# Kernel optimization log

Measured on AMD Instinct MI355X. Metric: run time of the kernel, lower is better.

Reference implementation:

```python
import jax, jax.numpy as jnp
import numpy as np

B, S, DIN, DOUT, A, T, H = 8, 1024, 1024, 1024, 4, 4, 8  # arity A, T cell types, hidden H


def setup_inputs() -> dict:
    key = jax.random.key(0)
    ks = jax.random.split(key, 6)
    x = jax.random.normal(ks[0], (B, S, DIN), jnp.float32)
    sc = 1.0 / np.sqrt(DIN).astype(np.float32)
    weight = jax.random.uniform(ks[1], (A * DOUT, DIN), jnp.float32, -sc, sc)
    bias = jax.random.uniform(ks[2], (A * DOUT,), jnp.float32, -sc, sc)
    # stacked per-cell-type MLP params: arity -> H -> 1 (tanh)
    cw1 = jax.random.normal(ks[3], (T, A, H), jnp.float32) / np.sqrt(A).astype(np.float32)
    cb1 = jnp.zeros((T, H), jnp.float32)
    cw2 = jax.random.normal(ks[4], (T, H), jnp.float32) / np.sqrt(H).astype(np.float32)
    cb2 = jnp.zeros((T,), jnp.float32)
    return {"x": x, "weight": weight, "bias": bias,
            "cw1": cw1, "cb1": cb1, "cw2": cw2, "cb2": cb2}


def reference(x, weight, bias, cw1, cb1, cw2, cb2):
    T_, A_, H_ = cw1.shape
    Dout = weight.shape[0] // A_
    G = Dout // T_  # neurons per cell type (cell_indices = contiguous blocks via np.repeat)
    # all_inputs = F.linear(input, weight, bias): (B, S, A*Dout)
    z = jnp.einsum('bsd,od->bso', x, weight) + bias
    # slice per-neuron arity chunks -> (B, S, T, G, A)
    z = z.reshape(z.shape[0], z.shape[1], T_, G, A_)
    # per-cell-type MLP applied to every neuron of that type (replaces Python loop)
    h = jnp.tanh(jnp.einsum('bstga,tah->bstgh', z, cw1) + cb1[:, None, :])
    o = jnp.einsum('bstgh,th->bstg', h, cw2) + cb2[:, None]
    # concat over neurons -> (B, S, Dout)
    return o.reshape(o.shape[0], o.shape[1], Dout)
```

## Files before the change

kernel.cpp:

```cpp
#include <hip/hip_runtime.h>


typedef __bf16 bf16x8 __attribute__((ext_vector_type(8)));
typedef float f32x4 __attribute__((ext_vector_type(4)));
typedef float f32x16 __attribute__((ext_vector_type(16)));

#define BM 256
#define BN 256
#define BK 64
#define KDIM 1024
#define NT 16
#define BUFB 65536
#define BBASE 32768
#define RS 321
#define XN8 (8192 * 1024 / 8)
#define WN8 (4096 * 1024 / 8)

__global__ __launch_bounds__(256) void cvt_bf16_kernel(
    const float* __restrict__ x, const float* __restrict__ w,
    __bf16* __restrict__ xb, __bf16* __restrict__ wb) {
    int i = blockIdx.x * 256 + threadIdx.x;
    const float* src;
    __bf16* dst;
    int j;
    if (i < XN8) { src = x; dst = xb; j = i; }
    else         { src = w; dst = wb; j = i - XN8; }
    const f32x4* p = (const f32x4*)src + 2 * (size_t)j;
    f32x4 a = p[0], b = p[1];
    bf16x8 o;
    o[0] = (__bf16)a[0]; o[1] = (__bf16)a[1]; o[2] = (__bf16)a[2]; o[3] = (__bf16)a[3];
    o[4] = (__bf16)b[0]; o[5] = (__bf16)b[1]; o[6] = (__bf16)b[2]; o[7] = (__bf16)b[3];
    ((bf16x8*)dst)[j] = o;
}

union __align__(16) SmemU {
    unsigned char raw[2 * BUFB];
    float z[64 * RS];
};

#define FENCE() asm volatile("" ::: "memory")
#define BARRIER() do { FENCE(); __builtin_amdgcn_s_barrier(); FENCE(); } while (0)

__global__ __launch_bounds__(512, 2) void fused_gemm_mlp_kernel(
    const __bf16* __restrict__ Ag,
    const __bf16* __restrict__ Bg,
    const float* __restrict__ bias,
    const float* __restrict__ cw1,
    const float* __restrict__ cb1,
    const float* __restrict__ cw2,
    const float* __restrict__ cb2,
    float* __restrict__ out)
{
    __shared__ SmemU u;

    const int tid  = threadIdx.x;
    const int wave = tid >> 6;
    const int lane = tid & 63;
    const int wm = wave >> 2;
    const int wn = wave & 3;
    const int bn0 = blockIdx.x * BN;
    const int bm0 = blockIdx.y * BM;

    const int srow  = lane >> 3;
    const int scol8 = (((lane & 7) ^ srow) * 8);

    const int lr5 = lane & 31;
    const int lk2 = lane >> 5;
    const int lx  = lane & 7;
    const int lg  = lr5 >> 3;
    int aoff[4], boff[2], slot[4];
#pragma unroll
    for (int mi = 0; mi < 4; ++mi) aoff[mi] = (wm * 16 + mi * 4 + lg) * 1024 + lx * 128;
#pragma unroll
    for (int ni = 0; ni < 2; ++ni) boff[ni] = BBASE + (wn * 8 + ni * 4 + lg) * 1024 + lx * 128;
#pragma unroll
    for (int ks = 0; ks < 4; ++ks) slot[ks] = ((ks * 2 + lk2) ^ lx) * 16;

    const char* sb = (const char*)u.raw;

    auto stageA = [&](int t, int half) {
        if (t >= NT) return;
        const int dst = (t & 1) * BUFB + (half * 16 + wave * 2) * 1024;
        const __bf16* g = Ag + (size_t)(bm0 + half * 128 + wave * 16 + srow) * KDIM
                        + t * BK + scol8;
        __builtin_amdgcn_global_load_lds(
            (__attribute__((address_space(1))) void*)g,
            (__attribute__((address_space(3))) void*)&u.raw[dst], 16, 0, 0);
        __builtin_amdgcn_global_load_lds(
            (__attribute__((address_space(1))) void*)(g + 8 * KDIM),
            (__attribute__((address_space(3))) void*)&u.raw[dst + 1024], 16, 0, 0);
    };
    auto stageB = [&](int t, int half) {
        if (t >= NT) return;
        const int dst = (t & 1) * BUFB + BBASE + (half * 16 + wave * 2) * 1024;
        const __bf16* g = Bg + (size_t)(bn0 + half * 128 + wave * 16 + srow) * KDIM
                        + t * BK + scol8;
        __builtin_amdgcn_global_load_lds(
            (__attribute__((address_space(1))) void*)g,
            (__attribute__((address_space(3))) void*)&u.raw[dst], 16, 0, 0);
        __builtin_amdgcn_global_load_lds(
            (__attribute__((address_space(1))) void*)(g + 8 * KDIM),
            (__attribute__((address_space(3))) void*)&u.raw[dst + 1024], 16, 0, 0);
    };

    f32x16 acc[4][2] = {};
    bf16x8 aA[8];
    bf16x8 a1f[8];
    bf16x8 bf0[4], bf1[4];

    stageA(0, 0); stageA(0, 1); stageB(0, 0); stageB(0, 1); stageB(1, 0);
    asm volatile("s_waitcnt vmcnt(2)" ::: "memory");
    BARRIER();
#pragma unroll
    for (int mi = 0; mi < 2; ++mi)
#pragma unroll
        for (int ks = 0; ks < 4; ++ks)
            aA[mi * 4 + ks] = *(const bf16x8*)(sb + aoff[mi] + slot[ks]);
#pragma unroll
    for (int ks = 0; ks < 4; ++ks)
        bf0[ks] = *(const bf16x8*)(sb + boff[0] + slot[ks]);
    stageB(1, 1);

#pragma unroll 2
    for (int T = 0; T < NT; ++T) {
        const int buf  = (T & 1) * BUFB;
        const int nbuf = buf ^ BUFB;

        BARRIER();
#pragma unroll
        for (int ks = 0; ks < 4; ++ks)
            bf1[ks] = *(const bf16x8*)(sb + buf + boff[1] + slot[ks]);
        stageA(T + 1, 0);
        __builtin_amdgcn_s_setprio(1);
#pragma unroll
        for (int mi = 0; mi < 2; ++mi)
#pragma unroll
            for (int ks = 0; ks < 4; ++ks)
                acc[mi][0] = __builtin_amdgcn_mfma_f32_32x32x16_bf16(
                    aA[mi * 4 + ks], bf0[ks], acc[mi][0], 0, 0, 0);
        __builtin_amdgcn_s_setprio(0);

        BARRIER();
#pragma unroll
        for (int mi = 0; mi < 2; ++mi)
#pragma unroll
            for (int ks = 0; ks < 4; ++ks)
                a1f[mi * 4 + ks] = *(const bf16x8*)(sb + buf + aoff[2 + mi] + slot[ks]);
        stageA(T + 1, 1);
        __builtin_amdgcn_s_setprio(1);
#pragma unroll
        for (int mi = 0; mi < 2; ++mi)
#pragma unroll
            for (int ks = 0; ks < 4; ++ks)
                acc[mi][1] = __builtin_amdgcn_mfma_f32_32x32x16_bf16(
                    aA[mi * 4 + ks], bf1[ks], acc[mi][1], 0, 0, 0);
        __builtin_amdgcn_s_setprio(0);

        BARRIER();
        stageB(T + 2, 0);
        __builtin_amdgcn_s_setprio(1);
#pragma unroll
        for (int mi = 0; mi < 2; ++mi)
#pragma unroll
            for (int ks = 0; ks < 4; ++ks)
                acc[2 + mi][0] = __builtin_amdgcn_mfma_f32_32x32x16_bf16(
                    a1f[mi * 4 + ks], bf0[ks], acc[2 + mi][0], 0, 0, 0);
        __builtin_amdgcn_s_setprio(0);
        if (T + 2 < NT) asm volatile("s_waitcnt vmcnt(2)" ::: "memory");
        else            asm volatile("s_waitcnt vmcnt(0)" ::: "memory");

        BARRIER();
        if (T + 1 < NT) {
#pragma unroll
            for (int mi = 0; mi < 2; ++mi)
#pragma unroll
                for (int ks = 0; ks < 4; ++ks)
                    aA[mi * 4 + ks] = *(const bf16x8*)(sb + nbuf + aoff[mi] + slot[ks]);
#pragma unroll
            for (int ks = 0; ks < 4; ++ks)
                bf0[ks] = *(const bf16x8*)(sb + nbuf + boff[0] + slot[ks]);
        }
        stageB(T + 2, 1);
        __builtin_amdgcn_s_setprio(1);
#pragma unroll
        for (int mi = 0; mi < 2; ++mi)
#pragma unroll
            for (int ks = 0; ks < 4; ++ks)
                acc[2 + mi][1] = __builtin_amdgcn_mfma_f32_32x32x16_bf16(
                    a1f[mi * 4 + ks], bf1[ks], acc[2 + mi][1], 0, 0, 0);
        __builtin_amdgcn_s_setprio(0);
    }

    const int tct = bn0 >> 10;
    float w1[32], b1[8], w2[8];
#pragma unroll
    for (int i = 0; i < 32; ++i) w1[i] = cw1[tct * 32 + i];
#pragma unroll
    for (int i = 0; i < 8; ++i) { b1[i] = cb1[tct * 8 + i]; w2[i] = cw2[tct * 8 + i]; }
    const float b2 = cb2[tct];

    float bcol[2];
    int zc[2];
#pragma unroll
    for (int ni = 0; ni < 2; ++ni) {
        const int n = wn * 64 + ni * 32 + lr5;
        bcol[ni] = bias[bn0 + n];
        zc[ni] = 5 * (n >> 2) + (n & 3);
    }

    const float L2E2 = 2.885390081777927f;

    asm volatile("s_waitcnt vmcnt(0)" ::: "memory");
    __syncthreads();

#pragma unroll
    for (int h = 0; h < 4; ++h) {
        if (wm == (h >> 1)) {
            const int mi0 = (h & 1) * 2;
#pragma unroll
            for (int dmi = 0; dmi < 2; ++dmi) {
#pragma unroll
                for (int ni = 0; ni < 2; ++ni) {
#pragma unroll
                    for (int g = 0; g < 4; ++g) {
                        const int rb = dmi * 32 + g * 8 + lk2 * 4;
                        u.z[(rb + 0) * RS + zc[ni]] = acc[mi0 + dmi][ni][g * 4 + 0] + bcol[ni];
                        u.z[(rb + 1) * RS + zc[ni]] = acc[mi0 + dmi][ni][g * 4 + 1] + bcol[ni];
                        u.z[(rb + 2) * RS + zc[ni]] = acc[mi0 + dmi][ni][g * 4 + 2] + bcol[ni];
                        u.z[(rb + 3) * RS + zc[ni]] = acc[mi0 + dmi][ni][g * 4 + 3] + bcol[ni];
                    }
                }
            }
        }
        __syncthreads();

#pragma unroll
        for (int it = 0; it < 8; ++it) {
            const int i = tid + it * 512;
            const int q = i & 63;
            const int r = i >> 6;
            const float* zp = &u.z[r * RS + 5 * q];
            const float z0 = zp[0], z1 = zp[1], z2 = zp[2], z3 = zp[3];
            float o = 0.f;
#pragma unroll
            for (int hh = 0; hh < 8; ++hh) {
                float pre = z0 * w1[0 * 8 + hh] + z1 * w1[1 * 8 + hh]
                          + z2 * w1[2 * 8 + hh] + z3 * w1[3 * 8 + hh] + b1[hh];
                float e = __builtin_amdgcn_exp2f(pre * L2E2);
                float th = 1.0f - 2.0f * __builtin_amdgcn_rcpf(e + 1.0f);
                o += th * w2[hh];
            }
            o += b2;
            out[(size_t)(bm0 + h * 64 + r) * 1024 + (bn0 >> 2) + q] = o;
        }
        __syncthreads();
    }
}

extern "C" void kernel_launch(void* const* d_in, const int* in_sizes, int n_in,
                              void* d_out, int out_size, void* d_ws, size_t ws_size,
                              hipStream_t stream) {
    const float* x    = (const float*)d_in[0];
    const float* w    = (const float*)d_in[1];
    const float* bias = (const float*)d_in[2];
    const float* cw1  = (const float*)d_in[3];
    const float* cb1  = (const float*)d_in[4];
    const float* cw2  = (const float*)d_in[5];
    const float* cb2  = (const float*)d_in[6];
    float* out = (float*)d_out;

    __bf16* xb = (__bf16*)d_ws;
    __bf16* wb = xb + (size_t)8192 * 1024;

    cvt_bf16_kernel<<<(XN8 + WN8) / 256, 256, 0, stream>>>(x, w, xb, wb);

    dim3 grid(4096 / BN, 8192 / BM);
    fused_gemm_mlp_kernel<<<grid, 512, 0, stream>>>(xb, wb, bias, cw1, cb1, cw2, cb2, out);
}
```

Before: 202.4 us.

## Prefetch A tiles two stages ahead alongside B in GEMM main loop

Reschedules the double-buffered main loop of the fused GEMM+MLP kernel. A-tile global-to-LDS loads are now issued for tile T+2 together with the B loads in the later phases, instead of for tile T+1 in the early phases. The fragment reads from LDS are also moved earlier, and the vmcnt/lgkmcnt waits are consolidated into the second phase. The aim is more lead time for global loads and better overlap of LDS reads with MFMA work. The cost is a full vmcnt(0) wait mid-iteration, and correctness now depends on buffer reuse ordering across the barriers.

```diff
diff --git a/kernel.cpp b/kernel.cpp
--- a/kernel.cpp
+++ b/kernel.cpp
@@ -40,6 +40,8 @@
 
 #define FENCE() asm volatile("" ::: "memory")
 #define BARRIER() do { FENCE(); __builtin_amdgcn_s_barrier(); FENCE(); } while (0)
+#define VMCNT(n) asm volatile("s_waitcnt vmcnt(" #n ")" ::: "memory")
+#define LGKM0()  asm volatile("s_waitcnt lgkmcnt(0)" ::: "memory")
 
 __global__ __launch_bounds__(512, 2) void fused_gemm_mlp_kernel(
     const __bf16* __restrict__ Ag,
@@ -108,18 +110,34 @@
     bf16x8 a1f[8];
     bf16x8 bf0[4], bf1[4];
 
-    stageA(0, 0); stageA(0, 1); stageB(0, 0); stageB(0, 1); stageB(1, 0);
-    asm volatile("s_waitcnt vmcnt(2)" ::: "memory");
+    auto readA = [&](bf16x8* dst, int base, int mi) {
+#pragma unroll
+        for (int ks = 0; ks < 4; ++ks)
+            dst[ks] = *(const bf16x8*)(sb + base + aoff[mi] + slot[ks]);
+    };
+    auto readB = [&](bf16x8* dst, int base, int ni) {
+#pragma unroll
+        for (int ks = 0; ks < 4; ++ks)
+            dst[ks] = *(const bf16x8*)(sb + base + boff[ni] + slot[ks]);
+    };
+    auto mmq = [&](const bf16x8* af, const bf16x8* bfr, int mq, int ni) {
+        __builtin_amdgcn_s_setprio(1);
+#pragma unroll
+        for (int mi = 0; mi < 2; ++mi)
+#pragma unroll
+            for (int ks = 0; ks < 4; ++ks)
+                acc[mq * 2 + mi][ni] = __builtin_amdgcn_mfma_f32_32x32x16_bf16(
+                    af[mi * 4 + ks], bfr[ks], acc[mq * 2 + mi][ni], 0, 0, 0);
+        __builtin_amdgcn_s_setprio(0);
+    };
+
+    stageA(0, 0); stageA(0, 1); stageB(0, 0); stageB(0, 1);
+    stageB(1, 0); stageA(1, 0);
+    VMCNT(4);
     BARRIER();
-#pragma unroll
-    for (int mi = 0; mi < 2; ++mi)
-#pragma unroll
-        for (int ks = 0; ks < 4; ++ks)
-            aA[mi * 4 + ks] = *(const bf16x8*)(sb + aoff[mi] + slot[ks]);
-#pragma unroll
-    for (int ks = 0; ks < 4; ++ks)
-        bf0[ks] = *(const bf16x8*)(sb + boff[0] + slot[ks]);
-    stageB(1, 1);
+    readA(aA, 0, 0); readA(aA + 4, 0, 1);
+    readB(bf0, 0, 0);
+    stageB(1, 1); stageA(1, 1);
 
 #pragma unroll 2
     for (int T = 0; T < NT; ++T) {
@@ -127,68 +145,27 @@
         const int nbuf = buf ^ BUFB;
 
         BARRIER();
-#pragma unroll
-        for (int ks = 0; ks < 4; ++ks)
-            bf1[ks] = *(const bf16x8*)(sb + buf + boff[1] + slot[ks]);
-        stageA(T + 1, 0);
-        __builtin_amdgcn_s_setprio(1);
-#pragma unroll
-        for (int mi = 0; mi < 2; ++mi)
-#pragma unroll
-            for (int ks = 0; ks < 4; ++ks)
-                acc[mi][0] = __builtin_amdgcn_mfma_f32_32x32x16_bf16(
-                    aA[mi * 4 + ks], bf0[ks], acc[mi][0], 0, 0, 0);
-        __builtin_amdgcn_s_setprio(0);
-
-        BARRIER();
-#pragma unroll
-        for (int mi = 0; mi < 2; ++mi)
-#pragma unroll
-            for (int ks = 0; ks < 4; ++ks)
-                a1f[mi * 4 + ks] = *(const bf16x8*)(sb + buf + aoff[2 + mi] + slot[ks]);
-        stageA(T + 1, 1);
-        __builtin_amdgcn_s_setprio(1);
-#pragma unroll
-        for (int mi = 0; mi < 2; ++mi)
-#pragma unroll
-            for (int ks = 0; ks < 4; ++ks)
-                acc[mi][1] = __builtin_amdgcn_mfma_f32_32x32x16_bf16(
-                    aA[mi * 4 + ks], bf1[ks], acc[mi][1], 0, 0, 0);
-        __builtin_amdgcn_s_setprio(0);
+        readB(bf1, buf, 1);
+        readA(a1f, buf, 2);
+        mmq(aA, bf0, 0, 0);
+
+        BARRIER();
+        readA(a1f + 4, buf, 3);
+        mmq(aA, bf1, 0, 1);
+        LGKM0();
+        VMCNT(0);
 
         BARRIER();
         stageB(T + 2, 0);
-        __builtin_amdgcn_s_setprio(1);
-#pragma unroll
-        for (int mi = 0; mi < 2; ++mi)
-#pragma unroll
-            for (int ks = 0; ks < 4; ++ks)
-                acc[2 + mi][0] = __builtin_amdgcn_mfma_f32_32x32x16_bf16(
-                    a1f[mi * 4 + ks], bf0[ks], acc[2 + mi][0], 0, 0, 0);
-        __builtin_amdgcn_s_setprio(0);
-        if (T + 2 < NT) asm volatile("s_waitcnt vmcnt(2)" ::: "memory");
-        else            asm volatile("s_waitcnt vmcnt(0)" ::: "memory");
-
-        BARRIER();
-        if (T + 1 < NT) {
-#pragma unroll
-            for (int mi = 0; mi < 2; ++mi)
-#pragma unroll
-                for (int ks = 0; ks < 4; ++ks)
-                    aA[mi * 4 + ks] = *(const bf16x8*)(sb + nbuf + aoff[mi] + slot[ks]);
-#pragma unroll
-            for (int ks = 0; ks < 4; ++ks)
-                bf0[ks] = *(const bf16x8*)(sb + nbuf + boff[0] + slot[ks]);
-        }
+        stageA(T + 2, 0);
+        if (T + 1 < NT) { readA(aA, nbuf, 0); readA(aA + 4, nbuf, 1); }
+        mmq(a1f, bf0, 1, 0);
+
+        BARRIER();
         stageB(T + 2, 1);
-        __builtin_amdgcn_s_setprio(1);
-#pragma unroll
-        for (int mi = 0; mi < 2; ++mi)
-#pragma unroll
-            for (int ks = 0; ks < 4; ++ks)
-                acc[2 + mi][1] = __builtin_amdgcn_mfma_f32_32x32x16_bf16(
-                    a1f[mi * 4 + ks], bf1[ks], acc[2 + mi][1], 0, 0, 0);
-        __builtin_amdgcn_s_setprio(0);
+        stageA(T + 2, 1);
+        if (T + 1 < NT) readB(bf0, nbuf, 0);
+        mmq(a1f, bf1, 1, 1);
     }
 
     const int tct = bn0 >> 10;
@@ -210,7 +187,6 @@
 
     const float L2E2 = 2.885390081777927f;
 
-    asm volatile("s_waitcnt vmcnt(0)" ::: "memory");
     __syncthreads();
 
 #pragma unroll
```

After: 196.7 us. -2.8%, faster.
